# Kernel optimization log

Measured on AMD Instinct MI355X. Metric: run time of the kernel, lower is better.

The kernel has to match this reference:

```python
import jax, jax.numpy as jnp
import numpy as np

DIM = 256
N_HEADS = 8
HEAD_DIM = DIM // N_HEADS
SCALE = HEAD_DIM ** -0.5
LN_EPS = 1e-5
SPIKE_NORM = 4.0  # MultiSpike/Multispike quantization level (Norm=4, standard in spike-driven transformer repos)


def multispike(x):
    """Integer multi-spike activation with straight-through estimator.
    forward: round(clip(x,0,4))/4 ; backward: identity on (0,4), 0 outside.
    Used both as the softmax replacement (spike1) and post-LN spike."""
    c = jnp.clip(x, 0.0, SPIKE_NORM) / SPIKE_NORM
    q = jnp.round(jnp.clip(x, 0.0, SPIKE_NORM)) / SPIKE_NORM
    return c + jax.lax.stop_gradient(q - c)


def layernorm(x, g, b):
    mu = jnp.mean(x, axis=-1, keepdims=True)
    var = jnp.var(x, axis=-1, keepdims=True)
    return (x - mu) * jax.lax.rsqrt(var + LN_EPS) * g + b


def setup_inputs() -> dict:
    key = jax.random.key(0)
    ks = jax.random.split(key, 8)
    B, C, H, W = 16, DIM, 128, 128
    feature_map = jax.random.normal(ks[0], (B, C, H, W), dtype=jnp.float32)
    audio_feature = jax.random.normal(ks[1], (B, 1, C), dtype=jnp.float32)
    s = 1.0 / np.sqrt(C)
    Wq = jax.random.uniform(ks[2], (C, C), jnp.float32, -s, s)
    Wkv = jax.random.uniform(ks[3], (2 * C, C), jnp.float32, -s, s)
    Wp = jax.random.uniform(ks[4], (C, C), jnp.float32, -s, s)
    bp = jax.random.uniform(ks[5], (C,), jnp.float32, -s, s)
    ln_g = jnp.ones((C,), jnp.float32)
    ln_b = jnp.zeros((C,), jnp.float32)
    return {"feature_map": feature_map, "audio_feature": audio_feature,
            "Wq": Wq, "Wkv": Wkv, "Wp": Wp, "bp": bp, "ln_g": ln_g, "ln_b": ln_b}


def reference(feature_map, audio_feature, Wq, Wkv, Wp, bp, ln_g, ln_b):
    B, C, H, W = feature_map.shape
    N = H * W
    flat = feature_map.reshape(B, C, N).transpose(0, 2, 1)  # (B, N, C)

    # q: (B,1,C) -> (B, heads, 1, d)
    q = (audio_feature @ Wq.T).reshape(B, 1, N_HEADS, HEAD_DIM).transpose(0, 2, 1, 3)
    kv = (flat @ Wkv.T).reshape(B, N, 2, N_HEADS, HEAD_DIM).transpose(2, 0, 3, 1, 4)
    k, v = kv[0], kv[1]

    attn = jnp.einsum('bhqd,bhkd->bhqk', q, k) * SCALE  # (B, heads, 1, N)
    attn = multispike(attn)  # spike activation replaces softmax
    x = jnp.einsum('bhqk,bhkd->bhqd', attn, v)          # (B, heads, 1, d)
    x = x.transpose(0, 2, 1, 3).reshape(B, 1, C)

    x = x @ Wp.T + bp
    x = layernorm(x, ln_g, ln_b)
    x = multispike(x)                                    # (B, 1, C)

    scale_bc = x[:, 0, :]                                # (B, C)
    fusion_map = feature_map * scale_bc[:, :, None, None]
    return fusion_map
```

## Files before the change

### kernel.cpp

```cpp
#include <hip/hip_runtime.h>
#include <math.h>

#define DIMC 256
#define NH 8
#define NPIX 16384
#define BATCH 16
#define ATT_SCALE 0.17677669529663687f
#define LN_EPS 1e-5f
#define NBLK_S 4

typedef float vfloat4 __attribute__((ext_vector_type(4)));

__global__ __launch_bounds__(256) void k_qk(const float* __restrict__ audio,
                                            const float* __restrict__ Wq,
                                            const float* __restrict__ Wkv,
                                            float* __restrict__ qkT) {
    const int blk = blockIdx.x;
    const int b   = blk >> 5;
    const int c0  = (blk & 31) * 8;
    const int t   = threadIdx.x;
    __shared__ float aud[DIMC];
    __shared__ float qL[DIMC];
    aud[t] = audio[b * DIMC + t];
    __syncthreads();
    {
        const float* wr = Wq + (size_t)t * DIMC;
        float acc = 0.f;
        for (int c = 0; c < DIMC; c += 4) {
            float4 w = *(const float4*)(wr + c);
            acc = fmaf(w.x, aud[c],     acc);
            acc = fmaf(w.y, aud[c + 1], acc);
            acc = fmaf(w.z, aud[c + 2], acc);
            acc = fmaf(w.w, aud[c + 3], acc);
        }
        qL[t] = acc;
    }
    __syncthreads();
    if (t < 64) {
        const int c = c0 + (t & 7);
        const int h = t >> 3;
        float acc = 0.f;
#pragma unroll
        for (int d = 0; d < 32; ++d)
            acc = fmaf(qL[h * 32 + d], Wkv[(size_t)(h * 32 + d) * DIMC + c], acc);
        qkT[((size_t)b * DIMC + c) * NH + h] = ATT_SCALE * acc;
    }
}

__global__ __launch_bounds__(256) void k_attn(const float* __restrict__ fm,
                                              const float* __restrict__ qkT,
                                              float* __restrict__ a) {
    int blk  = blockIdx.x;
    int b    = blk >> 5;
    int nblk = blk & 31;
    int t    = threadIdx.x;

    const int n0 = nblk * 512 + t * 2;
    const float* fmb = fm + (size_t)b * DIMC * NPIX + n0;
    const float* qb  = qkT + (size_t)b * DIMC * NH;

    float a0[NH], a1[NH];
#pragma unroll
    for (int h = 0; h < NH; ++h) { a0[h] = 0.f; a1[h] = 0.f; }

#pragma unroll 8
    for (int c = 0; c < DIMC; ++c) {
        float2 v  = *(const float2*)(fmb + (size_t)c * NPIX);
        float4 q0 = *(const float4*)(qb + c * NH);
        float4 q1 = *(const float4*)(qb + c * NH + 4);
        a0[0] = fmaf(v.x, q0.x, a0[0]); a1[0] = fmaf(v.y, q0.x, a1[0]);
        a0[1] = fmaf(v.x, q0.y, a0[1]); a1[1] = fmaf(v.y, q0.y, a1[1]);
        a0[2] = fmaf(v.x, q0.z, a0[2]); a1[2] = fmaf(v.y, q0.z, a1[2]);
        a0[3] = fmaf(v.x, q0.w, a0[3]); a1[3] = fmaf(v.y, q0.w, a1[3]);
        a0[4] = fmaf(v.x, q1.x, a0[4]); a1[4] = fmaf(v.y, q1.x, a1[4]);
        a0[5] = fmaf(v.x, q1.y, a0[5]); a1[5] = fmaf(v.y, q1.y, a1[5]);
        a0[6] = fmaf(v.x, q1.z, a0[6]); a1[6] = fmaf(v.y, q1.z, a1[6]);
        a0[7] = fmaf(v.x, q1.w, a0[7]); a1[7] = fmaf(v.y, q1.w, a1[7]);
    }

#pragma unroll
    for (int h = 0; h < NH; ++h) {
        float2 o;
        o.x = rintf(fminf(fmaxf(a0[h], 0.f), 4.f)) * 0.25f;
        o.y = rintf(fminf(fmaxf(a1[h], 0.f), 4.f)) * 0.25f;
        *(float2*)(a + ((size_t)b * NH + h) * NPIX + n0) = o;
    }
}

__global__ __launch_bounds__(256) void k_s(const float* __restrict__ fm,
                                           const float* __restrict__ a,
                                           float* __restrict__ s_part) {
    int d    = blockIdx.x;
    int blk  = (d & 7) * 128 + (d >> 3);
    int b    = blk >> 6;
    int nblk = (blk >> 4) & 3;
    int cblk = blk & 15;
    int t    = threadIdx.x;
    int c_l  = t >> 4;
    int nq   = t & 15;
    int c    = cblk * 16 + c_l;

    const float* fr = fm + ((size_t)b * DIMC + c) * NPIX + nblk * 4096 + nq * 4;
    const float* ab = a + (size_t)b * NH * NPIX + nblk * 4096 + nq * 4;

    float acc[NH];
#pragma unroll
    for (int h = 0; h < NH; ++h) acc[h] = 0.f;

#pragma unroll 2
    for (int j = 0; j < 64; ++j) {
        float4 v = *(const float4*)(fr + j * 64);
#pragma unroll
        for (int h = 0; h < NH; ++h) {
            float4 av = *(const float4*)(ab + (size_t)h * NPIX + j * 64);
            acc[h] += fmaf(v.x, av.x, fmaf(v.y, av.y, fmaf(v.z, av.z, v.w * av.w)));
        }
    }

    __shared__ float red[256 * NH];
#pragma unroll
    for (int h = 0; h < NH; ++h) red[t * NH + h] = acc[h];
    __syncthreads();

    if (t < 128) {
        int cl = t >> 3, h = t & 7;
        float sum = 0.f;
#pragma unroll
        for (int q = 0; q < 16; ++q)
            sum += red[(cl * 16 + q) * NH + h];
        s_part[(((size_t)b * NBLK_S + nblk) * NH + h) * DIMC + cblk * 16 + cl] = sum;
    }
}

__global__ __launch_bounds__(256) void k_scale(const float* __restrict__ s_part,
                                               const float* __restrict__ Wkv,
                                               const float* __restrict__ Wp,
                                               const float* __restrict__ bp,
                                               const float* __restrict__ g,
                                               const float* __restrict__ beta,
                                               float* __restrict__ scale) {
    int b = blockIdx.x;
    int t = threadIdx.x;
    __shared__ float sL[NH][DIMC];
    __shared__ float xL[DIMC];
    __shared__ float red[8];
    __shared__ float mu_s, var_s;

    for (int h = 0; h < NH; ++h) {
        float acc = 0.f;
        for (int sl = 0; sl < NBLK_S; ++sl)
            acc += s_part[(((size_t)b * NBLK_S + sl) * NH + h) * DIMC + t];
        sL[h][t] = acc;
    }
    __syncthreads();

    {
        const float* wr = Wkv + (size_t)(DIMC + t) * DIMC;
        const float* sr = sL[t >> 5];
        float acc = 0.f;
        for (int cc = 0; cc < DIMC; cc += 4) {
            float4 w = *(const float4*)(wr + cc);
            acc = fmaf(w.x, sr[cc],     acc);
            acc = fmaf(w.y, sr[cc + 1], acc);
            acc = fmaf(w.z, sr[cc + 2], acc);
            acc = fmaf(w.w, sr[cc + 3], acc);
        }
        xL[t] = acc;
    }
    __syncthreads();

    float p;
    {
        const float* wr = Wp + (size_t)t * DIMC;
        float acc = 0.f;
        for (int i = 0; i < DIMC; i += 4) {
            float4 w = *(const float4*)(wr + i);
            acc = fmaf(w.x, xL[i],     acc);
            acc = fmaf(w.y, xL[i + 1], acc);
            acc = fmaf(w.z, xL[i + 2], acc);
            acc = fmaf(w.w, xL[i + 3], acc);
        }
        p = acc + bp[t];
    }

    int lane = t & 63, wid = t >> 6;
    float r = p;
#pragma unroll
    for (int off = 32; off > 0; off >>= 1) r += __shfl_down(r, off);
    if (lane == 0) red[wid] = r;
    __syncthreads();
    if (t == 0) mu_s = (red[0] + red[1] + red[2] + red[3]) * (1.f / 256.f);
    __syncthreads();
    float mu = mu_s;
    float dd = p - mu;
    float r2 = dd * dd;
#pragma unroll
    for (int off = 32; off > 0; off >>= 1) r2 += __shfl_down(r2, off);
    if (lane == 0) red[4 + wid] = r2;
    __syncthreads();
    if (t == 0) var_s = (red[4] + red[5] + red[6] + red[7]) * (1.f / 256.f);
    __syncthreads();

    float ln = dd * (1.0f / sqrtf(var_s + LN_EPS)) * g[t] + beta[t];
    scale[b * DIMC + t] = rintf(fminf(fmaxf(ln, 0.f), 4.f)) * 0.25f;
}

__global__ __launch_bounds__(256) void k_out(const float* __restrict__ fm,
                                             const float* __restrict__ scale,
                                             float* __restrict__ out) {
    const size_t total4 = (size_t)BATCH * DIMC * NPIX / 4;
    const size_t tile   = 512;
    const size_t stride = (size_t)gridDim.x * tile;
    const int t = threadIdx.x;
    for (size_t base = (size_t)blockIdx.x * tile; base < total4; base += stride) {
        size_t i0 = base + t;
        size_t i1 = base + t + 256;
        vfloat4 v0 = *(const vfloat4*)(fm + i0 * 4);
        vfloat4 v1 = *(const vfloat4*)(fm + i1 * 4);
        float s0 = scale[i0 >> 12];
        float s1 = scale[i1 >> 12];
        vfloat4 o0 = v0 * s0;
        vfloat4 o1 = v1 * s1;
        __builtin_nontemporal_store(o0, (vfloat4*)(out + i0 * 4));
        __builtin_nontemporal_store(o1, (vfloat4*)(out + i1 * 4));
    }
}

extern "C" void kernel_launch(void* const* d_in, const int* in_sizes, int n_in,
                              void* d_out, int out_size, void* d_ws, size_t ws_size,
                              hipStream_t stream) {
    (void)in_sizes; (void)n_in; (void)out_size; (void)ws_size;
    const float* fm    = (const float*)d_in[0];
    const float* audio = (const float*)d_in[1];
    const float* Wq    = (const float*)d_in[2];
    const float* Wkv   = (const float*)d_in[3];
    const float* Wp    = (const float*)d_in[4];
    const float* bp    = (const float*)d_in[5];
    const float* g     = (const float*)d_in[6];
    const float* beta  = (const float*)d_in[7];
    float* out = (float*)d_out;

    char* ws = (char*)d_ws;
    float* qkT    = (float*)(ws);
    float* a      = (float*)(ws + (size_t)131072);
    float* s_part = (float*)(ws + (size_t)131072 + 8388608);
    float* scale  = (float*)(ws + (size_t)131072 + 8388608 + 524288);

    hipLaunchKernelGGL(k_qk,    dim3(512),        dim3(256), 0, stream, audio, Wq, Wkv, qkT);
    hipLaunchKernelGGL(k_attn,  dim3(512),        dim3(256), 0, stream, fm, qkT, a);
    hipLaunchKernelGGL(k_s,     dim3(1024),       dim3(256), 0, stream, fm, a, s_part);
    hipLaunchKernelGGL(k_scale, dim3(BATCH),      dim3(256), 0, stream, s_part, Wkv, Wp, bp, g, beta, scale);
    hipLaunchKernelGGL(k_out,   dim3(2048),       dim3(256), 0, stream, fm, scale, out);
}
```

Before: 239.2 us.

## Retile k_s to reuse attention vectors across four channels per thread

```diff
diff --git a/kernel.cpp b/kernel.cpp
--- a/kernel.cpp
+++ b/kernel.cpp
@@ -7,7 +7,7 @@
 #define BATCH 16
 #define ATT_SCALE 0.17677669529663687f
 #define LN_EPS 1e-5f
-#define NBLK_S 4
+#define NBLK_S 16
 
 typedef float vfloat4 __attribute__((ext_vector_type(4)));
 
@@ -90,45 +90,61 @@
 __global__ __launch_bounds__(256) void k_s(const float* __restrict__ fm,
                                            const float* __restrict__ a,
                                            float* __restrict__ s_part) {
-    int d    = blockIdx.x;
-    int blk  = (d & 7) * 128 + (d >> 3);
-    int b    = blk >> 6;
-    int nblk = (blk >> 4) & 3;
-    int cblk = blk & 15;
-    int t    = threadIdx.x;
-    int c_l  = t >> 4;
-    int nq   = t & 15;
-    int c    = cblk * 16 + c_l;
-
-    const float* fr = fm + ((size_t)b * DIMC + c) * NPIX + nblk * 4096 + nq * 4;
-    const float* ab = a + (size_t)b * NH * NPIX + nblk * 4096 + nq * 4;
-
-    float acc[NH];
-#pragma unroll
-    for (int h = 0; h < NH; ++h) acc[h] = 0.f;
+    const int d    = blockIdx.x;
+    const int blk  = (d & 7) * 128 + (d >> 3);
+    const int b    = blk >> 6;
+    const int nblk = (blk >> 2) & 15;
+    const int cq   = blk & 3;
+    const int t    = threadIdx.x;
+    const int cg   = t >> 4;
+    const int nq   = t & 15;
+    const int c0   = cq * 64 + cg * 4;
+    const int n0   = nblk * 1024;
+
+    const float* fr = fm + ((size_t)b * DIMC + c0) * NPIX + n0 + nq * 4;
+    const float* ab = a + (size_t)b * NH * NPIX + n0 + nq * 4;
+
+    float acc[4][NH];
+#pragma unroll
+    for (int k = 0; k < 4; ++k)
+#pragma unroll
+        for (int h = 0; h < NH; ++h) acc[k][h] = 0.f;
 
 #pragma unroll 2
-    for (int j = 0; j < 64; ++j) {
-        float4 v = *(const float4*)(fr + j * 64);
+    for (int j = 0; j < 16; ++j) {
+        float4 av[NH];
+#pragma unroll
+        for (int h = 0; h < NH; ++h)
+            av[h] = *(const float4*)(ab + (size_t)h * NPIX + j * 64);
+#pragma unroll
+        for (int k = 0; k < 4; ++k) {
+            float4 v = *(const float4*)(fr + (size_t)k * NPIX + j * 64);
+#pragma unroll
+            for (int h = 0; h < NH; ++h)
+                acc[k][h] += fmaf(v.x, av[h].x,
+                             fmaf(v.y, av[h].y,
+                             fmaf(v.z, av[h].z, v.w * av[h].w)));
+        }
+    }
+
+#pragma unroll
+    for (int k = 0; k < 4; ++k)
 #pragma unroll
         for (int h = 0; h < NH; ++h) {
-            float4 av = *(const float4*)(ab + (size_t)h * NPIX + j * 64);
-            acc[h] += fmaf(v.x, av.x, fmaf(v.y, av.y, fmaf(v.z, av.z, v.w * av.w)));
-        }
-    }
-
-    __shared__ float red[256 * NH];
-#pragma unroll
-    for (int h = 0; h < NH; ++h) red[t * NH + h] = acc[h];
-    __syncthreads();
-
-    if (t < 128) {
-        int cl = t >> 3, h = t & 7;
-        float sum = 0.f;
-#pragma unroll
-        for (int q = 0; q < 16; ++q)
-            sum += red[(cl * 16 + q) * NH + h];
-        s_part[(((size_t)b * NBLK_S + nblk) * NH + h) * DIMC + cblk * 16 + cl] = sum;
+            float x = acc[k][h];
+            x += __shfl_xor(x, 1);
+            x += __shfl_xor(x, 2);
+            x += __shfl_xor(x, 4);
+            x += __shfl_xor(x, 8);
+            acc[k][h] = x;
+        }
+
+    if (nq == 0) {
+#pragma unroll
+        for (int k = 0; k < 4; ++k)
+#pragma unroll
+            for (int h = 0; h < NH; ++h)
+                s_part[(((size_t)b * NBLK_S + nblk) * NH + h) * DIMC + c0 + k] = acc[k][h];
     }
 }
 
@@ -244,7 +260,7 @@
     float* qkT    = (float*)(ws);
     float* a      = (float*)(ws + (size_t)131072);
     float* s_part = (float*)(ws + (size_t)131072 + 8388608);
-    float* scale  = (float*)(ws + (size_t)131072 + 8388608 + 524288);
+    float* scale  = (float*)(ws + (size_t)131072 + 8388608 + 2097152);
 
     hipLaunchKernelGGL(k_qk,    dim3(512),        dim3(256), 0, stream, audio, Wq, Wkv, qkT);
     hipLaunchKernelGGL(k_attn,  dim3(512),        dim3(256), 0, stream, fm, qkT, a);
```

Measured after the change: 213.6 us. 10.7% less time.
